# Performance work log

Hardware: AMD Instinct MI355X
Metric: run time of the kernel (lower is better)

Reference implementation:

```python
import jax, jax.numpy as jnp
import numpy as np

B, C, H, W = 64, 256, 14, 14
K = 9
HID = 256   # EdgeAgg hidden_channels = in_channels
OUT = 512   # out_channels = 2*in_channels (required by final reshape)


def _knn(q, kset, k):
    # ViG dense_knn_matrix: squared-distance knn, top-k of -dist (self-loop may be included)
    qs = jnp.sum(q * q, -1)
    ks = jnp.sum(kset * kset, -1)
    dist = qs[:, :, None] - 2.0 * jnp.einsum('bnc,bmc->bnm', q, kset) + ks[:, None, :]
    _, idx = jax.lax.top_k(-dist, k)   # (B,N,k) neighbor indices into kset
    return idx


def _edgeconv_add(feat, nbr, validf, w, b):
    # PyG EdgeConv(nn=Linear, aggr='add') with per-node valid-edge mask:
    #   out[i] = sum_{j in valid nbrs(i)} cat(x_i, x_j - x_i) @ w + b
    # nn is linear, so aggregate neighbor diffs BEFORE the matmul (same math, less traffic).
    Cf = feat.shape[-1]
    wa, wb = w[:Cf], w[Cf:]
    deg = jnp.sum(validf, -1, keepdims=True)                   # (B,N,1)
    xj = feat[jnp.arange(feat.shape[0])[:, None, None], nbr]   # (B,N,k,C) gather
    sum_xj = jnp.einsum('bnkc,bnk->bnc', xj, validf)
    return deg * (feat @ wa + b) + (sum_xj - deg * feat) @ wb


def _forward(x, fc1_w, fc1_b, fc2_w, fc2_b, fce_w, fce_b, inout_w, inout_b,
             attn_w, attn_b, upd_w, upd_b, kp_w, kp_b, enc_w, enc_b,
             mu_w, mu_b, dec_w, dec_b, T):
    k = dec_w.shape[-1]
    b_, c_, h_, w_ = x.shape
    n = h_ * w_
    xs = x.reshape(b_, c_, n)                       # (B,C,N)
    x_sp = jnp.transpose(xs, (0, 2, 1))             # (B,N,C) true spatial node feats for knn
    x_sp_d = jax.lax.stop_gradient(x_sp)            # original detaches before knn
    x_nbr = _knn(x_sp_d, x_sp_d, k)
    # temporal roll across the T frames of each clip
    y_sp = jnp.roll(x_sp.reshape(b_ // T, T, n, c_), -1, axis=1).reshape(b_, n, c_)
    y_nbr = _knn(x_sp_d, jax.lax.stop_gradient(y_sp), k)
    # faithful to original: x.view(B*N, C) reinterprets the contiguous (B,C,N) buffer
    x_feat = xs.reshape(b_, n, c_)
    y_feat = jnp.transpose(y_sp, (0, 2, 1)).reshape(b_, n, c_)
    # VAE-like K predictor (deterministic z = mu); argmax -> per-node degree in [0,k)
    hk = x_feat.reshape(b_ * n, c_) @ kp_w + kp_b
    hk = jax.nn.relu(hk @ enc_w + enc_b)
    mu = hk @ mu_w + mu_b
    logits = mu @ dec_w + dec_b                     # (B*N, k)
    k_int = jnp.argmax(logits, axis=1)
    # generate_mask: keep the first k_int[i] of node i's k edges
    validf = (jnp.arange(k)[None, :] < k_int[:, None]).astype(x.dtype).reshape(b_, n, k)

    def edge_agg(feat, nbr):
        h1 = jax.nn.relu(_edgeconv_add(feat, nbr, validf, fc1_w, fc1_b))
        h2 = _edgeconv_add(h1, nbr, validf, fc2_w, fc2_b)
        return (h2 @ fce_w + fce_b).reshape(b_ * n, -1)

    x_agg = edge_agg(x_feat, x_nbr)
    y_agg = edge_agg(y_feat, y_nbr)
    scores = (jnp.concatenate([x_agg, y_agg], -1) @ attn_w + attn_b)[:, 0]
    wgt = jax.nn.softmax(scores, axis=0)[:, None]   # softmax over ALL B*N nodes (as in source)
    fused = wgt * x_agg + (1.0 - wgt) * y_agg
    xin = x_feat.reshape(b_ * n, c_) @ inout_w + inout_b
    upd = jax.nn.relu(jnp.concatenate([xin, fused], -1) @ upd_w + upd_b)   # (B*N, 2C)
    return jnp.transpose(upd.reshape(b_, n, 2 * c_), (0, 2, 1)).reshape(b_, 2 * c_, h_, w_)


def setup_inputs():
    key = jax.random.key(0)
    ks = iter(jax.random.split(key, 32))

    def lin(i, o):
        return jax.random.normal(next(ks), (i, o), jnp.float32) / np.sqrt(i)

    def bias(o):
        return jax.random.normal(next(ks), (o,), jnp.float32) * 0.01

    return {
        'x': jax.random.normal(next(ks), (B, C, H, W), jnp.float32),
        'fc1_w': lin(2 * C, HID), 'fc1_b': bias(HID),
        'fc2_w': lin(2 * HID, HID), 'fc2_b': bias(HID),
        'fce_w': lin(HID, OUT), 'fce_b': bias(OUT),
        'inout_w': lin(C, OUT), 'inout_b': bias(OUT),
        'attn_w': lin(2 * OUT, 1), 'attn_b': bias(1),
        'upd_w': lin(2 * OUT, OUT), 'upd_b': bias(OUT),
        'kp_w': lin(C, 500), 'kp_b': bias(500),
        'enc_w': lin(500, 64), 'enc_b': bias(64),
        'mu_w': lin(64, 32), 'mu_b': bias(32),
        'dec_w': lin(32, K), 'dec_b': bias(K),
        'T': 16,
    }


def reference(x, fc1_w, fc1_b, fc2_w, fc2_b, fce_w, fce_b, inout_w, inout_b,
              attn_w, attn_b, upd_w, upd_b, kp_w, kp_b, enc_w, enc_b,
              mu_w, mu_b, dec_w, dec_b, T):
    return _forward(x, fc1_w, fc1_b, fc2_w, fc2_b, fce_w, fce_b, inout_w, inout_b,
                    attn_w, attn_b, upd_w, upd_b, kp_w, kp_b, enc_w, enc_b,
                    mu_w, mu_b, dec_w, dec_b, T)
```

## Files before the change

### kernel.cpp

```cpp
#include <hip/hip_runtime.h>
#include <cstddef>
#include <cstdint>

constexpr int BATCH = 64;
constexpr int CH    = 256;
constexpr int NPT   = 196;
constexpr int ROWS  = BATCH * NPT;
constexpr int BSTRIDE = CH * NPT;
constexpr int KNB   = 8;

typedef __bf16 bf16x8 __attribute__((ext_vector_type(8)));
typedef __bf16 bf16x4 __attribute__((ext_vector_type(4)));
typedef _Float16 f16x8 __attribute__((ext_vector_type(8)));
typedef float  f32x4  __attribute__((ext_vector_type(4)));
typedef unsigned long long u64;

__device__ __forceinline__ int src_batch(int b) {
    return (b & ~15) | ((b + 1) & 15);
}

__device__ __forceinline__ void gload_lds16(const void* g, void* l) {
    __builtin_amdgcn_global_load_lds(
        (const __attribute__((address_space(1))) void*)g,
        (__attribute__((address_space(3))) void*)l, 16, 0, 0);
}

__device__ __forceinline__ int xcd_swz(int lin, int nwg) {
    int q = nwg >> 3;
    return (lin & 7) * q + (lin >> 3);
}

__global__ __launch_bounds__(256) void front_kernel(const float* __restrict__ x,
        _Float16* __restrict__ XH, _Float16* __restrict__ XL,
        __bf16* __restrict__ XB, float* __restrict__ qs,
        const float* __restrict__ W1, const float* __restrict__ b1,
        const float* __restrict__ W2, const float* __restrict__ b2,
        int* __restrict__ kint, float* __restrict__ degf) {
    __shared__ __attribute__((aligned(16))) char smem[21056];
    int bid = blockIdx.x;
    int t = threadIdx.x;
    if (bid < 1024) {
        float (*tile)[65] = (float(*)[65])smem;
        int m0 = (bid & 3) * 64, c0 = ((bid >> 2) & 3) * 64, b = bid >> 4;
        const float* xb = x + (size_t)b * BSTRIDE;
        #pragma unroll
        for (int s = 0; s < 16; ++s) {
            int idx = s * 256 + t;
            int cc = idx >> 6, mm = idx & 63;
            int m = m0 + mm;
            float v = (m < NPT) ? xb[(size_t)(c0 + cc) * NPT + m] : 0.f;
            tile[cc][mm] = v;
            if (m < NPT)
                XB[(size_t)b * BSTRIDE + (size_t)(c0 + cc) * NPT + m] = (__bf16)v;
        }
        __syncthreads();
        #pragma unroll
        for (int s = 0; s < 16; ++s) {
            int idx = s * 256 + t;
            int mm = idx >> 6, cc = idx & 63;
            float v = tile[cc][mm];
            _Float16 h = (_Float16)v;
            size_t off = ((size_t)b * 256 + (m0 + mm)) * 256 + c0 + cc;
            XH[off] = h;
            XL[off] = (_Float16)(v - (float)h);
        }
    } else if (bid < 1088) {
        int b = bid - 1024;
        int m = t;
        if (m >= NPT) return;
        const float* xb = x + (size_t)b * BSTRIDE;
        float acc = 0.f;
        for (int c = 0; c < CH; ++c) {
            float v = xb[c * NPT + m];
            acc = fmaf(v, v, acc);
        }
        qs[b * NPT + m] = acc;
    } else {
        float (*xr)[256] = (float(*)[256])smem;
        float (*ebuf)[64] = (float(*)[64])(smem + 16384);
        float (*lg)[9]   = (float(*)[9])(smem + 20480);
        int r0 = (bid - 1088) * 16;
        const float4* xg = (const float4*)(x + (size_t)r0 * 256);
        float4* xs = (float4*)&xr[0][0];
        #pragma unroll
        for (int s = 0; s < 4; ++s) xs[s * 256 + t] = xg[s * 256 + t];
        __syncthreads();
        int w = t >> 6, l = t & 63;
        {
            float bb = b1[l];
            float a0 = bb, a1 = bb, a2 = bb, a3 = bb;
            const float* x0 = xr[w * 4 + 0];
            const float* x1 = xr[w * 4 + 1];
            const float* x2 = xr[w * 4 + 2];
            const float* x3 = xr[w * 4 + 3];
            for (int c = 0; c < 256; ++c) {
                float wv = W1[c * 64 + l];
                a0 = fmaf(x0[c], wv, a0);
                a1 = fmaf(x1[c], wv, a1);
                a2 = fmaf(x2[c], wv, a2);
                a3 = fmaf(x3[c], wv, a3);
            }
            ebuf[w * 4 + 0][l] = fmaxf(a0, 0.f);
            ebuf[w * 4 + 1][l] = fmaxf(a1, 0.f);
            ebuf[w * 4 + 2][l] = fmaxf(a2, 0.f);
            ebuf[w * 4 + 3][l] = fmaxf(a3, 0.f);
        }
        __syncthreads();
        int rr = t >> 4, cc = t & 15;
        if (cc < 9) {
            float acc = b2[cc];
            for (int j = 0; j < 64; ++j)
                acc = fmaf(ebuf[rr][j], W2[j * 9 + cc], acc);
            lg[rr][cc] = acc;
        }
        __syncthreads();
        if (cc == 0) {
            float best = lg[rr][0];
            int bi = 0;
            #pragma unroll
            for (int j = 1; j < 9; ++j)
                if (lg[rr][j] > best) { best = lg[rr][j]; bi = j; }
            kint[r0 + rr] = bi;
            degf[r0 + rr] = (float)bi;
        }
    }
}

__global__ __launch_bounds__(256) void gram_mfma(const _Float16* __restrict__ XH,
        const _Float16* __restrict__ XL, const float* __restrict__ qs,
        u64* __restrict__ cand) {
    __shared__ __attribute__((aligned(16))) _Float16 Ah[128 * 64];
    __shared__ __attribute__((aligned(16))) _Float16 Al[128 * 64];
    __shared__ __attribute__((aligned(16))) _Float16 Bh[128 * 64];
    __shared__ __attribute__((aligned(16))) _Float16 Bl[128 * 64];
    int lin = blockIdx.x + 2 * blockIdx.y + 4 * blockIdx.z;
    int nid = xcd_swz(lin, 512);
    int bx = nid & 1, by = (nid >> 1) & 1;
    int job = nid >> 2;
    int qb = (job < 64) ? job : job - 64;
    int kb = (job < 64) ? qb : src_batch(qb);
    int t = threadIdx.x, w = t >> 6, l = t & 63;
    int r0 = by * 128, c0 = bx * 128;
    int lr = l & 15, lg = l >> 4;
    int wr = (w >> 1) * 64, wc = (w & 1) * 64;
    const _Float16* qh = XH + (size_t)qb * 65536;
    const _Float16* ql = XL + (size_t)qb * 65536;
    const _Float16* kh = XH + (size_t)kb * 65536;
    const _Float16* kl = XL + (size_t)kb * 65536;
    f32x4 acc[4][4] = {};
    for (int k0 = 0; k0 < 256; k0 += 64) {
        #pragma unroll
        for (int i = 0; i < 4; ++i) {
            int row = (w * 4 + i) * 8 + (l >> 3);
            int c8 = l & 7;
            size_t goA = (size_t)(r0 + row) * 256 + k0 + c8 * 8;
            size_t goB = (size_t)(c0 + row) * 256 + k0 + c8 * 8;
            gload_lds16(qh + goA, Ah + (w * 4 + i) * 512);
            gload_lds16(ql + goA, Al + (w * 4 + i) * 512);
            gload_lds16(kh + goB, Bh + (w * 4 + i) * 512);
            gload_lds16(kl + goB, Bl + (w * 4 + i) * 512);
        }
        asm volatile("s_waitcnt vmcnt(0)" ::: "memory");
        __syncthreads();
        #pragma unroll
        for (int ks = 0; ks < 2; ++ks) {
            f16x8 ah[4], al[4], bh[4], bl[4];
            #pragma unroll
            for (int mi = 0; mi < 4; ++mi) {
                ah[mi] = *(const f16x8*)(Ah + (wr + mi * 16 + lr) * 64 + ks * 32 + lg * 8);
                al[mi] = *(const f16x8*)(Al + (wr + mi * 16 + lr) * 64 + ks * 32 + lg * 8);
            }
            #pragma unroll
            for (int ni = 0; ni < 4; ++ni) {
                bh[ni] = *(const f16x8*)(Bh + (wc + ni * 16 + lr) * 64 + ks * 32 + lg * 8);
                bl[ni] = *(const f16x8*)(Bl + (wc + ni * 16 + lr) * 64 + ks * 32 + lg * 8);
            }
            #pragma unroll
            for (int mi = 0; mi < 4; ++mi)
                #pragma unroll
                for (int ni = 0; ni < 4; ++ni) {
                    acc[mi][ni] = __builtin_amdgcn_mfma_f32_16x16x32_f16(
                        ah[mi], bh[ni], acc[mi][ni], 0, 0, 0);
                    acc[mi][ni] = __builtin_amdgcn_mfma_f32_16x16x32_f16(
                        ah[mi], bl[ni], acc[mi][ni], 0, 0, 0);
                    acc[mi][ni] = __builtin_amdgcn_mfma_f32_16x16x32_f16(
                        al[mi], bh[ni], acc[mi][ni], 0, 0, 0);
                }
        }
        __syncthreads();
    }
    const float* qsq = qs + qb * NPT;
    const float* qsk = qs + kb * NPT;
    int tile = (c0 + wc) >> 6;
    float ksv[4];
    #pragma unroll
    for (int ni = 0; ni < 4; ++ni) {
        int col = c0 + wc + ni * 16 + lr;
        ksv[ni] = (col < NPT) ? qsk[col] : 0.f;
    }
    #pragma unroll
    for (int mi = 0; mi < 4; ++mi) {
        #pragma unroll
        for (int r = 0; r < 4; ++r) {
            int row = r0 + wr + mi * 16 + lg * 4 + r;
            bool rowvalid = row < NPT;
            float qq = rowvalid ? qsq[row] : 0.f;
            u64 key[4];
            #pragma unroll
            for (int ni = 0; ni < 4; ++ni) {
                int col = c0 + wc + ni * 16 + lr;
                float dist = qq - 2.f * acc[mi][ni][r] + ksv[ni];
                unsigned u = __float_as_uint(dist);
                u = (u & 0x80000000u) ? ~u : (u | 0x80000000u);
                key[ni] = (col < NPT) ? (((u64)u << 32) | (unsigned)col) : ~0ull;
            }
            u64 outk[8];
            #pragma unroll
            for (int it = 0; it < 8; ++it) {
                u64 best = key[0];
                #pragma unroll
                for (int ni = 1; ni < 4; ++ni)
                    best = (key[ni] < best) ? key[ni] : best;
                #pragma unroll
                for (int m = 1; m <= 8; m <<= 1) {
                    u64 o = __shfl_xor(best, m, 64);
                    if (o < best) best = o;
                }
                outk[it] = best;
                #pragma unroll
                for (int ni = 0; ni < 4; ++ni)
                    if (key[ni] == best) key[ni] = ~0ull;
            }
            if (rowvalid && lr == 0) {
                u64* cp = cand + (((size_t)job * NPT + row) * 4 + tile) * 8;
                #pragma unroll
                for (int it = 0; it < 8; ++it) cp[it] = outk[it];
            }
        }
    }
}

__global__ __launch_bounds__(256) void topk_merge(const u64* __restrict__ cand,
                                                  int* __restrict__ nbr) {
    int rowid = blockIdx.x * 256 + threadIdx.x;
    const u64* c = cand + (size_t)rowid * 32;
    int p0 = 0, p1 = 0, p2 = 0, p3 = 0;
    #pragma unroll
    for (int it = 0; it < 8; ++it) {
        u64 v0 = c[p0], v1 = c[8 + p1], v2 = c[16 + p2], v3 = c[24 + p3];
        u64 best = v0; int bj = 0;
        if (v1 < best) { best = v1; bj = 1; }
        if (v2 < best) { best = v2; bj = 2; }
        if (v3 < best) { best = v3; bj = 3; }
        if (bj == 0) p0 = (p0 < 7) ? p0 + 1 : 7;
        else if (bj == 1) p1 = (p1 < 7) ? p1 + 1 : 7;
        else if (bj == 2) p2 = (p2 < 7) ? p2 + 1 : 7;
        else p3 = (p3 < 7) ? p3 + 1 : 7;
        nbr[(size_t)rowid * KNB + it] = (int)(best & 0xffffffffu);
    }
}

__global__ __launch_bounds__(256) void prep_weights(
        const float* __restrict__ fc1_w, const float* __restrict__ fc2_w,
        const float* __restrict__ fce_w, const float* __restrict__ upd_w,
        const float* __restrict__ kp_w, const float* __restrict__ kp_b,
        const float* __restrict__ enc_w, const float* __restrict__ enc_b,
        const float* __restrict__ mu_w, const float* __restrict__ mu_b,
        const float* __restrict__ dec_w, const float* __restrict__ dec_b,
        const float* __restrict__ inout_w, const float* __restrict__ inout_b,
        const float* __restrict__ upd_b,
        __bf16* __restrict__ W1catT, __bf16* __restrict__ W2catT,
        __bf16* __restrict__ fcet, __bf16* __restrict__ updC,
        float* __restrict__ KW1, float* __restrict__ kb1,
        float* __restrict__ KW2, float* __restrict__ kb2,
        float* __restrict__ bcomp) {
    __shared__ float tile[64][65];
    int bid = blockIdx.x;
    int t = threadIdx.x;
    if (bid < 64) {
        const float* W = (bid < 32) ? fc1_w : fc2_w;
        __bf16* WT = (bid < 32) ? W1catT : W2catT;
        int local = bid & 31;
        int n0 = (local >> 2) * 64, k0 = (local & 3) * 64;
        #pragma unroll
        for (int s = 0; s < 16; ++s) {
            int idx = s * 256 + t;
            int kk = idx >> 6, nn = idx & 63;
            float v;
            if (n0 < 256)
                v = W[(size_t)(k0 + kk) * 256 + n0 + nn] -
                    W[(size_t)(k0 + kk + 256) * 256 + n0 + nn];
            else
                v = W[(size_t)(k0 + kk + 256) * 256 + (n0 - 256) + nn];
            tile[kk][nn] = v;
        }
        __syncthreads();
        #pragma unroll
        for (int s = 0; s < 16; ++s) {
            int idx = s * 256 + t;
            int nn = idx >> 6, kk = idx & 63;
            WT[(size_t)(n0 + nn) * 256 + k0 + kk] = (__bf16)tile[kk][nn];
        }
    } else if (bid < 96) {
        int local = bid - 64;
        int n0 = (local >> 2) * 64, k0 = (local & 3) * 64;
        #pragma unroll
        for (int s = 0; s < 16; ++s) {
            int idx = s * 256 + t;
            int kk = idx >> 6, nn = idx & 63;
            tile[kk][nn] = fce_w[(size_t)(k0 + kk) * 512 + n0 + nn];
        }
        __syncthreads();
        #pragma unroll
        for (int s = 0; s < 16; ++s) {
            int idx = s * 256 + t;
            int nn = idx >> 6, kk = idx & 63;
            fcet[(size_t)(n0 + nn) * 256 + k0 + kk] = (__bf16)tile[kk][nn];
        }
    } else if (bid < 160) {
        int local = bid - 96;
        int k0 = (local >> 3) * 64, n0 = (local & 7) * 64;
        #pragma unroll
        for (int s = 0; s < 16; ++s) {
            int idx = s * 256 + t;
            int kk = idx >> 6, nn = idx & 63;
            tile[kk][nn] = upd_w[(size_t)(512 + k0 + kk) * 512 + n0 + nn];
        }
        __syncthreads();
        #pragma unroll
        for (int s = 0; s < 16; ++s) {
            int idx = s * 256 + t;
            int nn = idx >> 6, kk = idx & 63;
            updC[(size_t)(n0 + nn) * 768 + 256 + k0 + kk] = (__bf16)tile[kk][nn];
        }
    } else if (bid < 224) {
        int i = (bid - 160) * 4 + (t >> 6);
        int j = t & 63;
        double acc = 0.0;
        for (int k = 0; k < 500; ++k)
            acc += (double)kp_w[(size_t)i * 500 + k] * (double)enc_w[(size_t)k * 64 + j];
        KW1[i * 64 + j] = (float)acc;
    } else if (bid == 224) {
        int j = t;
        if (j < 64) {
            double acc = (double)enc_b[j];
            for (int k = 0; k < 500; ++k)
                acc += (double)kp_b[k] * (double)enc_w[(size_t)k * 64 + j];
            kb1[j] = (float)acc;
        }
    } else if (bid < 228) {
        int e = (bid - 225) * 256 + t;
        if (e < 576) {
            int i = e / 9, j = e - (e / 9) * 9;
            double acc = 0.0;
            for (int k = 0; k < 32; ++k)
                acc += (double)mu_w[(size_t)i * 32 + k] * (double)dec_w[(size_t)k * 9 + j];
            KW2[e] = (float)acc;
        } else if (e < 585) {
            int j = e - 576;
            double acc = (double)dec_b[j];
            for (int k = 0; k < 32; ++k)
                acc += (double)mu_b[k] * (double)dec_w[(size_t)k * 9 + j];
            kb2[j] = (float)acc;
        }
    } else if (bid < 740) {
        int e = (bid - 228) * 256 + t;
        int k = e >> 9, n = e & 511;
        double acc = 0.0;
        for (int j = 0; j < 512; ++j)
            acc += (double)inout_w[(size_t)k * 512 + j] * (double)upd_w[(size_t)j * 512 + n];
        updC[(size_t)n * 768 + k] = (__bf16)(float)acc;
    } else {
        int n = (bid - 740) * 256 + t;
        double acc = (double)upd_b[n];
        for (int j = 0; j < 512; ++j)
            acc += (double)inout_b[j] * (double)upd_w[(size_t)j * 512 + n];
        bcomp[n] = (float)acc;
    }
}

template<int STAGE, int RELU>
__global__ __launch_bounds__(256) void combine_kernel(const __bf16* __restrict__ P,
        const int* __restrict__ nbr, const int* __restrict__ kint_,
        const float* __restrict__ degf, const float* __restrict__ bias,
        __bf16* __restrict__ H) {
    int g = threadIdx.x >> 6, lane = threadIdx.x & 63;
    int nid = xcd_swz(blockIdx.x, 2 * ROWS / 4);
    int r = nid * 4 + g;
    int branch = (r >= ROWS);
    int rr = r - branch * ROWS;
    int b = rr / NPT, i = rr - b * NPT;
    size_t srow, mbase;
    if constexpr (STAGE == 1) {
        int fb = branch ? src_batch(b) : b;
        srow = (size_t)fb * NPT + i;
        mbase = (size_t)fb * NPT;
    } else {
        srow = (size_t)r;
        mbase = (size_t)branch * ROWS + (size_t)b * NPT;
    }
    const int* nb = nbr + (size_t)branch * ((size_t)ROWS * KNB) + (size_t)rr * KNB;
    bf16x4 sv = *(const bf16x4*)(P + srow * 512 + lane * 4);
    float4 bv = *(const float4*)(bias + lane * 4);
    float s0 = 0.f, s1 = 0.f, s2 = 0.f, s3 = 0.f;
    int kk = kint_[rr];
    for (int tt = 0; tt < kk; ++tt) {
        int m = nb[tt];
        bf16x4 v = *(const bf16x4*)(P + (mbase + m) * 512 + 256 + lane * 4);
        s0 += (float)v[0]; s1 += (float)v[1]; s2 += (float)v[2]; s3 += (float)v[3];
    }
    float dg = degf[rr];
    float o0 = fmaf(dg, (float)sv[0] + bv.x, s0);
    float o1 = fmaf(dg, (float)sv[1] + bv.y, s1);
    float o2 = fmaf(dg, (float)sv[2] + bv.z, s2);
    float o3 = fmaf(dg, (float)sv[3] + bv.w, s3);
    if constexpr (RELU) {
        o0 = fmaxf(o0, 0.f); o1 = fmaxf(o1, 0.f);
        o2 = fmaxf(o2, 0.f); o3 = fmaxf(o3, 0.f);
    }
    bf16x4 ov;
    ov[0] = (__bf16)o0; ov[1] = (__bf16)o1; ov[2] = (__bf16)o2; ov[3] = (__bf16)o3;
    *(bf16x4*)(H + (size_t)r * 256 + lane * 4) = ov;
}

template<int FLAGS, int CONCAT>
__global__ __launch_bounds__(256) void mfma_gemm(
    const __bf16* __restrict__ A0, const __bf16* __restrict__ A1,
    const __bf16* __restrict__ WT, const float* __restrict__ bias,
    float* __restrict__ Cf, __bf16* __restrict__ Cb, int K, int N,
    const float* __restrict__ aw, float* __restrict__ scp,
    const float* __restrict__ wgt) {
    constexpr int SMEMB = (FLAGS & 8) ? (128 * 129 * 4) : (2 * 128 * 64 * 2);
    __shared__ __attribute__((aligned(16))) char smem[SMEMB];
    __bf16* As = (__bf16*)smem;
    __bf16* Bs = As + 128 * 64;
    int lin = blockIdx.x + 4 * blockIdx.y;
    int nid = xcd_swz(lin, 4 * gridDim.y);
    int bx = nid & 3, by = nid >> 2;
    int t = threadIdx.x, w = t >> 6, l = t & 63;
    int r0 = by * 128, c0 = bx * 128;
    int lr = l & 15, lg = l >> 4;
    int wr = (w >> 1) * 64, wc = (w & 1) * 64;
    f32x4 acc[4][4] = {};
    for (int k0 = 0; k0 < K; k0 += 64) {
        #pragma unroll
        for (int i = 0; i < 4; ++i) {
            int row = (w * 4 + i) * 8 + (l >> 3);
            int c8 = l & 7;
            if constexpr (CONCAT == 2) {
                if (k0 < 256) {
                    gload_lds16(A0 + (size_t)(r0 + row) * 256 + k0 + c8 * 8,
                                As + (w * 4 + i) * 512);
                } else {
                    int kk2 = k0 - 256 + c8 * 8;
                    size_t gr = (size_t)(r0 + row);
                    bf16x8 xa = *(const bf16x8*)(A1 + gr * 512 + kk2);
                    bf16x8 ya = *(const bf16x8*)(A1 + ((size_t)ROWS + gr) * 512 + kk2);
                    float wv = wgt[gr];
                    bf16x8 mx;
                    #pragma unroll
                    for (int j = 0; j < 8; ++j)
                        mx[j] = (__bf16)(wv * (float)xa[j] + (1.f - wv) * (float)ya[j]);
                    *(bf16x8*)(As + (w * 4 + i) * 512 + l * 8) = mx;
                }
            } else {
                gload_lds16(A0 + (size_t)(r0 + row) * K + k0 + c8 * 8,
                            As + (w * 4 + i) * 512);
            }
            gload_lds16(WT + (size_t)(c0 + row) * K + k0 + c8 * 8,
                        Bs + (w * 4 + i) * 512);
        }
        asm volatile("s_waitcnt vmcnt(0)" ::: "memory");
        __syncthreads();
        #pragma unroll
        for (int ks = 0; ks < 2; ++ks) {
            bf16x8 af[4], bfr[4];
            #pragma unroll
            for (int mi = 0; mi < 4; ++mi)
                af[mi] = *(const bf16x8*)(As + (wr + mi * 16 + lr) * 64 + ks * 32 + lg * 8);
            #pragma unroll
            for (int ni = 0; ni < 4; ++ni)
                bfr[ni] = *(const bf16x8*)(Bs + (wc + ni * 16 + lr) * 64 + ks * 32 + lg * 8);
            #pragma unroll
            for (int mi = 0; mi < 4; ++mi)
                #pragma unroll
                for (int ni = 0; ni < 4; ++ni)
                    acc[mi][ni] = __builtin_amdgcn_mfma_f32_16x16x32_bf16(
                        af[mi], bfr[ni], acc[mi][ni], 0, 0, 0);
        }
        __syncthreads();
    }
    if constexpr ((FLAGS & 8) != 0) {
        float* tile = (float*)smem;
        #pragma unroll
        for (int mi = 0; mi < 4; ++mi)
            #pragma unroll
            for (int r = 0; r < 4; ++r) {
                int rrow = wr + mi * 16 + lg * 4 + r;
                #pragma unroll
                for (int ni = 0; ni < 4; ++ni) {
                    int ccol = wc + ni * 16 + lr;
                    float v = acc[mi][ni][r];
                    if (bias) v += bias[c0 + ccol];
                    if constexpr ((FLAGS & 1) != 0) v = fmaxf(v, 0.f);
                    tile[rrow * 129 + ccol] = v;
                }
            }
        __syncthreads();
        int cc = t >> 6, rr2 = t & 63;
        #pragma unroll
        for (int cs = 0; cs < 128; cs += 4) {
            #pragma unroll
            for (int h = 0; h < 2; ++h) {
                int row = r0 + rr2 + h * 64;
                int bb = row / NPT, ii = row - bb * NPT;
                Cf[((size_t)bb * 512 + (c0 + cc + cs)) * NPT + ii] =
                    tile[(rr2 + h * 64) * 129 + cc + cs];
            }
        }
    } else if constexpr ((FLAGS & 16) != 0) {
        int half = (r0 >= ROWS) ? 1 : 0;
        float ps[4][4] = {};
        #pragma unroll
        for (int mi = 0; mi < 4; ++mi)
            #pragma unroll
            for (int r = 0; r < 4; ++r) {
                int row = r0 + wr + mi * 16 + lg * 4 + r;
                #pragma unroll
                for (int ni = 0; ni < 4; ++ni) {
                    int col = c0 + wc + ni * 16 + lr;
                    float v = acc[mi][ni][r] + bias[col];
                    Cb[(size_t)row * N + col] = (__bf16)v;
                    ps[mi][r] = fmaf(v, aw[half * 512 + col], ps[mi][r]);
                }
            }
        #pragma unroll
        for (int m = 1; m <= 8; m <<= 1)
            #pragma unroll
            for (int mi = 0; mi < 4; ++mi)
                #pragma unroll
                for (int r = 0; r < 4; ++r)
                    ps[mi][r] += __shfl_xor(ps[mi][r], m, 64);
        if (lr == 0) {
            int slot = half * 8 + bx * 2 + (w & 1);
            #pragma unroll
            for (int mi = 0; mi < 4; ++mi)
                #pragma unroll
                for (int r = 0; r < 4; ++r) {
                    int sr = r0 - half * ROWS + wr + mi * 16 + lg * 4 + r;
                    scp[(size_t)slot * ROWS + sr] = ps[mi][r];
                }
        }
    } else {
        #pragma unroll
        for (int mi = 0; mi < 4; ++mi) {
            #pragma unroll
            for (int r = 0; r < 4; ++r) {
                int row = r0 + wr + mi * 16 + lg * 4 + r;
                #pragma unroll
                for (int ni = 0; ni < 4; ++ni) {
                    int col = c0 + wc + ni * 16 + lr;
                    float v = acc[mi][ni][r];
                    if (bias) v += bias[col];
                    if constexpr ((FLAGS & 1) != 0) v = fmaxf(v, 0.f);
                    if constexpr ((FLAGS & 4) != 0)
                        Cb[(size_t)row * N + col] = (__bf16)v;
                    else
                        Cf[(size_t)row * N + col] = v;
                }
            }
        }
    }
}

__global__ __launch_bounds__(256) void softmax_part(const float* __restrict__ scp,
        const float* __restrict__ ab, float* __restrict__ scores,
        float* __restrict__ mpart, float* __restrict__ spart) {
    __shared__ float red[256];
    int t = threadIdx.x;
    int sr = blockIdx.x * 256 + t;
    float s = ab[0];
    #pragma unroll
    for (int i = 0; i < 16; ++i) s += scp[(size_t)i * ROWS + sr];
    scores[sr] = s;
    red[t] = s; __syncthreads();
    for (int off = 128; off; off >>= 1) {
        if (t < off) red[t] = fmaxf(red[t], red[t + off]);
        __syncthreads();
    }
    float mb = red[0]; __syncthreads();
    red[t] = expf(s - mb); __syncthreads();
    for (int off = 128; off; off >>= 1) {
        if (t < off) red[t] += red[t + off];
        __syncthreads();
    }
    if (t == 0) { mpart[blockIdx.x] = mb; spart[blockIdx.x] = red[0]; }
}

__global__ __launch_bounds__(256) void softmax_fin(const float* __restrict__ mpart,
        const float* __restrict__ spart, const float* __restrict__ scores,
        float* __restrict__ wgt) {
    __shared__ float MS[2];
    if (threadIdx.x == 0) {
        float M = mpart[0];
        for (int i = 1; i < 49; ++i) M = fmaxf(M, mpart[i]);
        float S = 0.f;
        for (int i = 0; i < 49; ++i) S += spart[i] * expf(mpart[i] - M);
        MS[0] = M; MS[1] = S;
    }
    __syncthreads();
    float M = MS[0], denom = MS[1];
    for (int i = threadIdx.x; i < ROWS; i += 256)
        wgt[i] = expf(scores[i] - M) / denom;
}

extern "C" void kernel_launch(void* const* d_in, const int* in_sizes, int n_in,
                              void* d_out, int out_size, void* d_ws, size_t ws_size,
                              hipStream_t stream) {
    (void)in_sizes; (void)n_in; (void)out_size; (void)ws_size;
    const float* x       = (const float*)d_in[0];
    const float* fc1_w   = (const float*)d_in[1];
    const float* fc1_b   = (const float*)d_in[2];
    const float* fc2_w   = (const float*)d_in[3];
    const float* fc2_b   = (const float*)d_in[4];
    const float* fce_w   = (const float*)d_in[5];
    const float* fce_b   = (const float*)d_in[6];
    const float* inout_w = (const float*)d_in[7];
    const float* inout_b = (const float*)d_in[8];
    const float* attn_w  = (const float*)d_in[9];
    const float* attn_b  = (const float*)d_in[10];
    const float* upd_w   = (const float*)d_in[11];
    const float* upd_b   = (const float*)d_in[12];
    const float* kp_w    = (const float*)d_in[13];
    const float* kp_b    = (const float*)d_in[14];
    const float* enc_w   = (const float*)d_in[15];
    const float* enc_b   = (const float*)d_in[16];
    const float* mu_w    = (const float*)d_in[17];
    const float* mu_b    = (const float*)d_in[18];
    const float* dec_w   = (const float*)d_in[19];
    const float* dec_b   = (const float*)d_in[20];
    float* out = (float*)d_out;

    char* base = (char*)d_ws;
    size_t o = 0;
    auto alloc = [&](size_t bytes) -> void* {
        void* p = base + o;
        o += (bytes + 255) & ~(size_t)255;
        return p;
    };
    float* qs     = (float*)alloc(ROWS * 4);
    float* degf   = (float*)alloc(ROWS * 4);
    float* scores = (float*)alloc(ROWS * 4);
    float* wgt    = (float*)alloc(ROWS * 4);
    int*   kint   = (int*)  alloc(ROWS * 4);
    float* KW1    = (float*)alloc(256 * 64 * 4);
    float* kb1    = (float*)alloc(64 * 4);
    float* KW2    = (float*)alloc(64 * 9 * 4);
    float* kb2    = (float*)alloc(9 * 4);
    float* bcomp  = (float*)alloc(512 * 4);
    float* scp    = (float*)alloc((size_t)16 * ROWS * 4);
    float* mpart  = (float*)alloc(64 * 4);
    float* spart  = (float*)alloc(64 * 4);
    int*   nbr    = (int*)  alloc((size_t)128 * NPT * KNB * 4);
    u64*   cand   = (u64*)  alloc((size_t)128 * NPT * 4 * 8 * 8);
    char*  regD   = (char*) alloc((size_t)ROWS * 512 * 2);
    __bf16* XB    = (__bf16*)alloc((size_t)ROWS * 256 * 2);
    __bf16* H1    = (__bf16*)alloc((size_t)2 * ROWS * 256 * 2);
    __bf16* H2    = (__bf16*)alloc((size_t)2 * ROWS * 256 * 2);
    char*  regAGG = (char*) alloc((size_t)2 * ROWS * 512 * 4);
    __bf16* W1catT= (__bf16*)alloc((size_t)512 * 256 * 2);
    __bf16* W2catT= (__bf16*)alloc((size_t)512 * 256 * 2);
    __bf16* fcet  = (__bf16*)alloc((size_t)512 * 256 * 2);
    __bf16* updC  = (__bf16*)alloc((size_t)512 * 768 * 2);
    __bf16* P1buf = (__bf16*)regD;
    _Float16* XSPH = (_Float16*)regAGG;
    _Float16* XSPL = XSPH + (size_t)64 * 256 * 256;
    __bf16* P2buf = (__bf16*)regAGG;
    __bf16* AGGb  = (__bf16*)regAGG;
    __bf16* XAGGb = AGGb;

    prep_weights<<<742, 256, 0, stream>>>(fc1_w, fc2_w, fce_w, upd_w,
                                          kp_w, kp_b, enc_w, enc_b,
                                          mu_w, mu_b, dec_w, dec_b,
                                          inout_w, inout_b, upd_b,
                                          W1catT, W2catT, fcet, updC,
                                          KW1, kb1, KW2, kb2, bcomp);
    front_kernel<<<1872, 256, 0, stream>>>(x, XSPH, XSPL, XB, qs,
                                           KW1, kb1, KW2, kb2, kint, degf);

    gram_mfma<<<dim3(2, 2, 128), 256, 0, stream>>>(XSPH, XSPL, qs, cand);
    topk_merge<<<98, 256, 0, stream>>>(cand, nbr);

    mfma_gemm<4, 0><<<dim3(4, 98), 256, 0, stream>>>(
        XB, nullptr, W1catT, nullptr, nullptr, P1buf, 256, 512,
        nullptr, nullptr, nullptr);
    combine_kernel<1, 1><<<2 * ROWS / 4, 256, 0, stream>>>(
        P1buf, nbr, kint, degf, fc1_b, H1);

    mfma_gemm<4, 0><<<dim3(4, 196), 256, 0, stream>>>(
        H1, nullptr, W2catT, nullptr, nullptr, P2buf, 256, 512,
        nullptr, nullptr, nullptr);
    combine_kernel<2, 0><<<2 * ROWS / 4, 256, 0, stream>>>(
        P2buf, nbr, kint, degf, fc2_b, H2);

    mfma_gemm<20, 0><<<dim3(4, 196), 256, 0, stream>>>(
        H2, nullptr, fcet, fce_b, nullptr, AGGb, 256, 512,
        attn_w, scp, nullptr);

    softmax_part<<<49, 256, 0, stream>>>(scp, attn_b, scores, mpart, spart);
    softmax_fin<<<1, 256, 0, stream>>>(mpart, spart, scores, wgt);

    mfma_gemm<9, 2><<<dim3(4, 98), 256, 0, stream>>>(
        XB, XAGGb, updC, bcomp, out, nullptr, 768, 512,
        nullptr, nullptr, wgt);
}
```

Baseline: 242.8 us.

## Stage distances in LDS and do per-thread insertion top-8 instead of shuffle reductions

The gram kernel epilogue previously ran an 8-round wave-shuffle min-reduction for every row across 16 lanes. It now writes the distance tile to shared memory, reusing the operand buffers with a padded stride. Each thread then scans one 64-column half-row and keeps a sorted top-8 in registers via insertion. This removes many 64-bit shuffles, at the cost of an LDS round-trip, an extra barrier, serial per-thread scanning with branch divergence, and higher register use.

```diff
diff --git a/kernel.cpp b/kernel.cpp
--- a/kernel.cpp
+++ b/kernel.cpp
@@ -129,10 +129,12 @@
 __global__ __launch_bounds__(256) void gram_mfma(const _Float16* __restrict__ XH,
         const _Float16* __restrict__ XL, const float* __restrict__ qs,
         u64* __restrict__ cand) {
-    __shared__ __attribute__((aligned(16))) _Float16 Ah[128 * 64];
-    __shared__ __attribute__((aligned(16))) _Float16 Al[128 * 64];
-    __shared__ __attribute__((aligned(16))) _Float16 Bh[128 * 64];
-    __shared__ __attribute__((aligned(16))) _Float16 Bl[128 * 64];
+    __shared__ __attribute__((aligned(16))) char smem[128 * 132 * 4];
+    _Float16* Ah = (_Float16*)smem;
+    _Float16* Al = Ah + 128 * 64;
+    _Float16* Bh = Al + 128 * 64;
+    _Float16* Bl = Bh + 128 * 64;
+    float* dst = (float*)smem;
     int lin = blockIdx.x + 2 * blockIdx.y + 4 * blockIdx.z;
     int nid = xcd_swz(lin, 512);
     int bx = nid & 1, by = (nid >> 1) & 1;
@@ -191,7 +193,6 @@
     }
     const float* qsq = qs + qb * NPT;
     const float* qsk = qs + kb * NPT;
-    int tile = (c0 + wc) >> 6;
     float ksv[4];
     #pragma unroll
     for (int ni = 0; ni < 4; ++ni) {
@@ -202,40 +203,47 @@
     for (int mi = 0; mi < 4; ++mi) {
         #pragma unroll
         for (int r = 0; r < 4; ++r) {
-            int row = r0 + wr + mi * 16 + lg * 4 + r;
-            bool rowvalid = row < NPT;
-            float qq = rowvalid ? qsq[row] : 0.f;
-            u64 key[4];
+            int lrow = wr + mi * 16 + lg * 4 + r;
+            int grow = r0 + lrow;
+            float qq = (grow < NPT) ? qsq[grow] : 0.f;
             #pragma unroll
             for (int ni = 0; ni < 4; ++ni) {
-                int col = c0 + wc + ni * 16 + lr;
                 float dist = qq - 2.f * acc[mi][ni][r] + ksv[ni];
-                unsigned u = __float_as_uint(dist);
-                u = (u & 0x80000000u) ? ~u : (u | 0x80000000u);
-                key[ni] = (col < NPT) ? (((u64)u << 32) | (unsigned)col) : ~0ull;
-            }
-            u64 outk[8];
-            #pragma unroll
-            for (int it = 0; it < 8; ++it) {
-                u64 best = key[0];
+                dst[lrow * 132 + wc + ni * 16 + lr] = dist;
+            }
+        }
+    }
+    __syncthreads();
+    {
+        int lrow = t >> 1, half = t & 1;
+        int grow = r0 + lrow;
+        if (grow < NPT) {
+            int tile = (c0 >> 6) + half;
+            u64 kreg[8];
+            #pragma unroll
+            for (int p = 0; p < 8; ++p) kreg[p] = ~0ull;
+            const float* rp = dst + lrow * 132 + half * 64;
+            for (int s4 = 0; s4 < 16; ++s4) {
+                f32x4 dv = *(const f32x4*)(rp + s4 * 4);
                 #pragma unroll
-                for (int ni = 1; ni < 4; ++ni)
-                    best = (key[ni] < best) ? key[ni] : best;
-                #pragma unroll
-                for (int m = 1; m <= 8; m <<= 1) {
-                    u64 o = __shfl_xor(best, m, 64);
-                    if (o < best) best = o;
+                for (int e = 0; e < 4; ++e) {
+                    int col = (tile << 6) + s4 * 4 + e;
+                    unsigned u = __float_as_uint(dv[e]);
+                    u = (u & 0x80000000u) ? ~u : (u | 0x80000000u);
+                    u64 key = (col < NPT) ? (((u64)u << 32) | (unsigned)col) : ~0ull;
+                    if (key < kreg[7]) {
+                        #pragma unroll
+                        for (int p = 0; p < 8; ++p) {
+                            u64 mn = (key < kreg[p]) ? key : kreg[p];
+                            u64 mx = (key < kreg[p]) ? kreg[p] : key;
+                            kreg[p] = mn; key = mx;
+                        }
+                    }
                 }
-                outk[it] = best;
-                #pragma unroll
-                for (int ni = 0; ni < 4; ++ni)
-                    if (key[ni] == best) key[ni] = ~0ull;
-            }
-            if (rowvalid && lr == 0) {
-                u64* cp = cand + (((size_t)job * NPT + row) * 4 + tile) * 8;
-                #pragma unroll
-                for (int it = 0; it < 8; ++it) cp[it] = outk[it];
-            }
+            }
+            u64* cp = cand + (((size_t)job * NPT + grow) * 4 + tile) * 8;
+            #pragma unroll
+            for (int p = 0; p < 8; ++p) cp[p] = kreg[p];
         }
     }
 }
```

Result: no change. 241.5 us (-0.6%).
